# Kernel optimization log

Hardware: AMD Instinct MI355X
Metric: run time of the kernel (lower is better)

Reference implementation:

```python
import jax, jax.numpy as jnp
import numpy as np

IN_CH = 256
OUT_CH = 64
HEADS = 8


def setup_inputs() -> dict:
    key = jax.random.key(0)
    ks = jax.random.split(key, 7)
    N = 4096
    proj = OUT_CH * HEADS
    s_in = 1.0 / np.sqrt(IN_CH)
    return {
        "query_input": jax.random.normal(ks[0], (N, IN_CH), dtype=jnp.float32),
        "Wq": jax.random.uniform(ks[1], (proj, IN_CH), jnp.float32, -s_in, s_in),
        "bq": jax.random.uniform(ks[2], (proj,), jnp.float32, -s_in, s_in),
        "Wk": jax.random.uniform(ks[3], (proj, IN_CH), jnp.float32, -s_in, s_in),
        "bk": jax.random.uniform(ks[4], (proj,), jnp.float32, -s_in, s_in),
        "Wv": jax.random.uniform(ks[5], (proj, IN_CH), jnp.float32, -s_in, s_in),
        "bv": jax.random.uniform(ks[6], (proj,), jnp.float32, -s_in, s_in),
    }


def reference(query_input, Wq, bq, Wk, bk, Wv, bv):
    N = query_input.shape[0]
    # projections -> [N, H, M]
    q = (query_input @ Wq.T + bq).reshape(N, HEADS, OUT_CH)
    k = (query_input @ Wk.T + bk).reshape(N, HEADS, OUT_CH)
    v = (query_input @ Wv.T + bv).reshape(N, HEADS, OUT_CH)
    # sigmoid attention scores [N, L, H]
    attention_num = jax.nn.sigmoid(jnp.einsum('nhm,lhm->nlh', q, k))
    # sum-normalization over L (keys)
    normalizer = attention_num.sum(axis=1, keepdims=True)  # [N, 1, H]
    attention = attention_num / normalizer
    # weighted V reduction [N, H, D], then mean over heads -> [N, D]
    out = jnp.einsum('nlh,lhd->nhd', attention, v).mean(axis=1)
    return out
```

## Files before the change

### kernel.cpp

```cpp
#include <hip/hip_runtime.h>
#include <hip/hip_bf16.h>
#include <math.h>

#define N_TOK 4096
#define IN_CH 256
#define OUT_CH 64
#define HEADS 8
#define PROJ (OUT_CH * HEADS)
#define NLOG2E -1.44269504088896340736f

typedef float f32x4 __attribute__((ext_vector_type(4)));
typedef __bf16 bf16x8 __attribute__((ext_vector_type(8)));
typedef unsigned short ushort_t;

__device__ inline ushort_t bf16rne(float x) {
    unsigned u = __float_as_uint(x);
    unsigned r = (u + 0x7FFFu + ((u >> 16) & 1u)) >> 16;
    return (ushort_t)r;
}

__global__ __launch_bounds__(256) void cast_pack_kernel(
    const float* __restrict__ X,
    const float* __restrict__ Wq, const float* __restrict__ Wk,
    const float* __restrict__ Wv,
    ushort_t* __restrict__ Xa, ushort_t* __restrict__ Wp)
{
    const int i = blockIdx.x * 256 + threadIdx.x;
    const float* src;
    ushort_t* dst;
    float scale = 1.0f;
    if (i < 131072) {
        const int t = i & 15, quad = (i >> 4) & 3, k8 = (i >> 6) & 7, g = i >> 9;
        src = X + (size_t)(g * 16 + t) * IN_CH + k8 * 32 + quad * 8;
        dst = Xa + (size_t)i * 8;
    } else {
        const int j = i - 131072;
        const int z = j >> 14;
        const int r = j & 16383;
        const int cl = r & 15, quad = (r >> 4) & 3, k8 = (r >> 6) & 7, gc = r >> 9;
        const float* W = (z == 0) ? Wq : (z == 1) ? Wk : Wv;
        src = W + (size_t)(gc * 16 + cl) * IN_CH + k8 * 32 + quad * 8;
        dst = Wp + (size_t)z * 131072 * 8 + (size_t)r * 8;
        if (z == 0) scale = NLOG2E;
    }
    float4 a = *(const float4*)src;
    float4 b = *(const float4*)(src + 4);
    ushort_t pk[8];
    pk[0] = bf16rne(a.x * scale); pk[1] = bf16rne(a.y * scale);
    pk[2] = bf16rne(a.z * scale); pk[3] = bf16rne(a.w * scale);
    pk[4] = bf16rne(b.x * scale); pk[5] = bf16rne(b.y * scale);
    pk[6] = bf16rne(b.z * scale); pk[7] = bf16rne(b.w * scale);
    *(uint4*)dst = *(uint4*)pk;
}

__global__ __launch_bounds__(256) void proj_mfma_kernel(
    const ushort_t* __restrict__ Xa, const ushort_t* __restrict__ Wp,
    const float* __restrict__ bq, const float* __restrict__ bk,
    const float* __restrict__ bv,
    ushort_t* __restrict__ Qb, ushort_t* __restrict__ Kb,
    ushort_t* __restrict__ Vt)
{
    const int z = blockIdx.z;
    const float* bias = (z == 0) ? bq : (z == 1) ? bk : bv;
    const float bscale = (z == 0) ? NLOG2E : 1.0f;
    const int c0 = blockIdx.x * 64;
    const int n0 = blockIdx.y * 64;

    const int tid = threadIdx.x;
    const int w = tid >> 6;
    const int lane = tid & 63;
    const int l15 = lane & 15;
    const int quad = lane >> 4;

    __shared__ ushort_t Es[64 * 68];

    const ushort_t* xa = Xa + (size_t)(blockIdx.y * 4 + w) * 4096 + quad * 128 + l15 * 8;
    const ushort_t* wp0 = Wp + (size_t)z * 131072 * 8 +
                          (size_t)(blockIdx.x * 4) * 4096 + quad * 128 + l15 * 8;

    f32x4 acc[4] = {{0.f, 0.f, 0.f, 0.f}, {0.f, 0.f, 0.f, 0.f},
                    {0.f, 0.f, 0.f, 0.f}, {0.f, 0.f, 0.f, 0.f}};

#pragma unroll 2
    for (int k8 = 0; k8 < 8; ++k8) {
        bf16x8 a = *(const bf16x8*)(xa + k8 * 512);
#pragma unroll
        for (int f = 0; f < 4; ++f) {
            bf16x8 b = *(const bf16x8*)(wp0 + f * 4096 + k8 * 512);
            acc[f] = __builtin_amdgcn_mfma_f32_16x16x32_bf16(a, b, acc[f], 0, 0, 0);
        }
    }

    if (z < 2) {
#pragma unroll
        for (int f = 0; f < 4; ++f) {
            const float bb = bias[c0 + f * 16 + l15] * bscale;
#pragma unroll
            for (int r = 0; r < 4; ++r)
                Es[(w * 16 + quad * 4 + r) * 68 + f * 16 + l15] = bf16rne(acc[f][r] + bb);
        }
    } else {
#pragma unroll
        for (int f = 0; f < 4; ++f) {
            const float bb = bias[c0 + f * 16 + l15];
#pragma unroll
            for (int r = 0; r < 4; ++r)
                Es[(f * 16 + l15) * 68 + w * 16 + quad * 4 + r] = bf16rne(acc[f][r] + bb);
        }
    }
    __syncthreads();

    const int erow = tid >> 2;
    const int ecol = (tid & 3) * 16;
    uint4 pk0 = *(uint4*)&Es[erow * 68 + ecol];
    uint4 pk1 = *(uint4*)&Es[erow * 68 + ecol + 8];
    if (z < 2) {
        ushort_t* out = z ? Kb : Qb;
        ushort_t* p = &out[(size_t)(n0 + erow) * PROJ + c0 + ecol];
        *(uint4*)p = pk0;
        *(uint4*)(p + 8) = pk1;
    } else {
        ushort_t* p = &Vt[(size_t)(c0 + erow) * N_TOK + n0 + ecol];
        *(uint4*)p = pk0;
        *(uint4*)(p + 8) = pk1;
    }
}

__global__ __launch_bounds__(256, 4) void attn_kernel(
    const ushort_t* __restrict__ Qb, const ushort_t* __restrict__ Kb,
    const ushort_t* __restrict__ Vt,
    float* __restrict__ NUM, float* __restrict__ DEN)
{
    const int h = blockIdx.y;
    const int z = blockIdx.z;
    const int n0 = blockIdx.x * 64;
    const int tid = threadIdx.x;
    const int w = tid >> 6;
    const int lane = tid & 63;
    const int l15 = lane & 15;
    const int quad = lane >> 4;

    __shared__ ushort_t Ks[64 * 64];
    __shared__ ushort_t Vs[64 * 64];
    __shared__ ushort_t Ps[4][16 * 72];

    bf16x8 qb[2];
    {
        const ushort_t* base = Qb + (size_t)(n0 + w * 16 + l15) * PROJ + h * 64 + quad * 8;
        qb[0] = *(const bf16x8*)(base);
        qb[1] = *(const bf16x8*)(base + 32);
    }

    bf16x8 onesv;
#pragma unroll
    for (int j = 0; j < 8; ++j) onesv[j] = (__bf16)1.0f;

    f32x4 o[4] = {{0.f, 0.f, 0.f, 0.f}, {0.f, 0.f, 0.f, 0.f},
                  {0.f, 0.f, 0.f, 0.f}, {0.f, 0.f, 0.f, 0.f}};
    f32x4 dacc = {0.f, 0.f, 0.f, 0.f};

    const int srow = tid >> 2;
    const int sc2 = (tid & 3) * 2;
    const int sp0 = (sc2 ^ (srow & 7)) * 8;
    const int sp1 = ((sc2 + 1) ^ (srow & 7)) * 8;
    const int xm = l15 & 7;
    const int rofA = (quad ^ xm) * 8;
    const int rofB = ((4 + quad) ^ xm) * 8;

    const ushort_t* kgp = Kb + (size_t)h * 64 + sc2 * 8 +
                          (size_t)(z * 2048 + srow) * PROJ;
    const ushort_t* vgp = Vt + (size_t)h * 64 * N_TOK + (size_t)srow * N_TOK +
                          sc2 * 8 + z * 2048;

    uint4 kr0 = ((const uint4*)kgp)[0], kr1 = ((const uint4*)kgp)[1];
    uint4 vr0 = ((const uint4*)vgp)[0], vr1 = ((const uint4*)vgp)[1];

    for (int lt = 0; lt < 32; ++lt) {
        __syncthreads();
        *(uint4*)&Ks[srow * 64 + sp0] = kr0;
        *(uint4*)&Ks[srow * 64 + sp1] = kr1;
        *(uint4*)&Vs[srow * 64 + sp0] = vr0;
        *(uint4*)&Vs[srow * 64 + sp1] = vr1;
        __syncthreads();

        if (lt < 31) {
            kgp += 64 * PROJ;
            vgp += 64;
            kr0 = ((const uint4*)kgp)[0]; kr1 = ((const uint4*)kgp)[1];
            vr0 = ((const uint4*)vgp)[0]; vr1 = ((const uint4*)vgp)[1];
        }

        f32x4 s[4] = {{0.f, 0.f, 0.f, 0.f}, {0.f, 0.f, 0.f, 0.f},
                      {0.f, 0.f, 0.f, 0.f}, {0.f, 0.f, 0.f, 0.f}};
#pragma unroll
        for (int f = 0; f < 4; ++f) {
            bf16x8 ka = *(const bf16x8*)&Ks[(f * 16 + l15) * 64 + rofA];
            s[f] = __builtin_amdgcn_mfma_f32_16x16x32_bf16(ka, qb[0], s[f], 0, 0, 0);
        }
#pragma unroll
        for (int f = 0; f < 4; ++f) {
            bf16x8 ka = *(const bf16x8*)&Ks[(f * 16 + l15) * 64 + rofB];
            s[f] = __builtin_amdgcn_mfma_f32_16x16x32_bf16(ka, qb[1], s[f], 0, 0, 0);
        }

        ushort_t* pw = &Ps[w][l15 * 72];
#pragma unroll
        for (int f = 0; f < 4; ++f) {
            float p0 = __builtin_amdgcn_rcpf(1.0f + __builtin_amdgcn_exp2f(s[f][0]));
            float p1 = __builtin_amdgcn_rcpf(1.0f + __builtin_amdgcn_exp2f(s[f][1]));
            float p2 = __builtin_amdgcn_rcpf(1.0f + __builtin_amdgcn_exp2f(s[f][2]));
            float p3 = __builtin_amdgcn_rcpf(1.0f + __builtin_amdgcn_exp2f(s[f][3]));
            unsigned u0 = __float_as_uint(p0) + 0x8000u;
            unsigned u1 = __float_as_uint(p1) + 0x8000u;
            unsigned u2 = __float_as_uint(p2) + 0x8000u;
            unsigned u3 = __float_as_uint(p3) + 0x8000u;
            uint2 pk;
            pk.x = __builtin_amdgcn_perm(u1, u0, 0x07060302u);
            pk.y = __builtin_amdgcn_perm(u3, u2, 0x07060302u);
            *(uint2*)&pw[f * 16 + quad * 4] = pk;
        }

#pragma unroll
        for (int c = 0; c < 2; ++c) {
            bf16x8 pa = *(const bf16x8*)&Ps[w][l15 * 72 + c * 32 + quad * 8];
            const int rof = c ? rofB : rofA;
#pragma unroll
            for (int f = 0; f < 4; ++f) {
                bf16x8 vb = *(const bf16x8*)&Vs[(f * 16 + l15) * 64 + rof];
                o[f] = __builtin_amdgcn_mfma_f32_16x16x32_bf16(pa, vb, o[f], 0, 0, 0);
            }
            dacc = __builtin_amdgcn_mfma_f32_16x16x32_bf16(pa, onesv, dacc, 0, 0, 0);
        }
    }

#pragma unroll
    for (int f = 0; f < 4; ++f) {
#pragma unroll
        for (int r = 0; r < 4; ++r) {
            const int q = n0 + w * 16 + quad * 4 + r;
            NUM[((size_t)z * N_TOK + q) * PROJ + h * 64 + f * 16 + l15] = o[f][r];
        }
    }
    if (l15 == 0) {
#pragma unroll
        for (int r = 0; r < 4; ++r)
            DEN[((size_t)z * N_TOK + n0 + w * 16 + quad * 4 + r) * HEADS + h] = dacc[r];
    }
}

__global__ __launch_bounds__(256) void reduce_kernel(
    const float* __restrict__ NUM, const float* __restrict__ DEN,
    float* __restrict__ out)
{
    const int g = blockIdx.x * 256 + threadIdx.x;
    const int n = g >> 6;
    const int d = g & 63;
    float acc = 0.0f;
#pragma unroll
    for (int hh = 0; hh < HEADS; ++hh) {
        float num = NUM[(size_t)n * PROJ + hh * 64 + d] +
                    NUM[((size_t)N_TOK + n) * PROJ + hh * 64 + d];
        float dd = DEN[(size_t)n * HEADS + hh] +
                   DEN[((size_t)N_TOK + n) * HEADS + hh];
        acc += num / dd;
    }
    out[g] = acc * 0.125f;
}

extern "C" void kernel_launch(void* const* d_in, const int* in_sizes, int n_in,
                              void* d_out, int out_size, void* d_ws, size_t ws_size,
                              hipStream_t stream) {
    (void)in_sizes; (void)n_in; (void)out_size; (void)ws_size;
    const float* X  = (const float*)d_in[0];
    const float* Wq = (const float*)d_in[1];
    const float* bq = (const float*)d_in[2];
    const float* Wk = (const float*)d_in[3];
    const float* bk = (const float*)d_in[4];
    const float* Wv = (const float*)d_in[5];
    const float* bv = (const float*)d_in[6];
    float* out = (float*)d_out;

    float* NUM = (float*)d_ws;
    float* DEN = NUM + (size_t)2 * N_TOK * PROJ;
    ushort_t* Qb = (ushort_t*)(DEN + (size_t)2 * N_TOK * HEADS);
    ushort_t* Kb = Qb + (size_t)N_TOK * PROJ;
    ushort_t* Vt = Kb + (size_t)N_TOK * PROJ;
    ushort_t* Xa = Vt + (size_t)N_TOK * PROJ;
    ushort_t* Wp = Xa + (size_t)N_TOK * IN_CH;

    cast_pack_kernel<<<dim3(704), 256, 0, stream>>>(X, Wq, Wk, Wv, Xa, Wp);
    proj_mfma_kernel<<<dim3(PROJ / 64, N_TOK / 64, 3), 256, 0, stream>>>(
        Xa, Wp, bq, bk, bv, Qb, Kb, Vt);
    attn_kernel<<<dim3(N_TOK / 64, HEADS, 2), 256, 0, stream>>>(
        Qb, Kb, Vt, NUM, DEN);
    reduce_kernel<<<dim3(N_TOK * OUT_CH / 256), 256, 0, stream>>>(NUM, DEN, out);
}
```

Baseline: 142.9 us.

## Split attention keys four ways when workspace allows and raise MFMA wave priority

Templates the attention and reduce kernels on the number of key splits and picks four splits instead of two when the workspace is large enough. This doubles the grid to 2048 blocks and halves each block's key loop, so more blocks are in flight to hide latency. It also wraps the MFMA sections in s_setprio so matrix work gets issued ahead of other waves. The cost is twice as much partial NUM/DEN traffic to write and then reduce.

```diff
diff --git a/kernel.cpp b/kernel.cpp
--- a/kernel.cpp
+++ b/kernel.cpp
@@ -126,11 +126,15 @@
     }
 }
 
+template<int ZS>
 __global__ __launch_bounds__(256, 4) void attn_kernel(
     const ushort_t* __restrict__ Qb, const ushort_t* __restrict__ Kb,
     const ushort_t* __restrict__ Vt,
     float* __restrict__ NUM, float* __restrict__ DEN)
 {
+    constexpr int KEYS = N_TOK / ZS;
+    constexpr int TILES = KEYS / 64;
+
     const int h = blockIdx.y;
     const int z = blockIdx.z;
     const int n0 = blockIdx.x * 64;
@@ -168,14 +172,14 @@
     const int rofB = ((4 + quad) ^ xm) * 8;
 
     const ushort_t* kgp = Kb + (size_t)h * 64 + sc2 * 8 +
-                          (size_t)(z * 2048 + srow) * PROJ;
+                          (size_t)(z * KEYS + srow) * PROJ;
     const ushort_t* vgp = Vt + (size_t)h * 64 * N_TOK + (size_t)srow * N_TOK +
-                          sc2 * 8 + z * 2048;
+                          sc2 * 8 + z * KEYS;
 
     uint4 kr0 = ((const uint4*)kgp)[0], kr1 = ((const uint4*)kgp)[1];
     uint4 vr0 = ((const uint4*)vgp)[0], vr1 = ((const uint4*)vgp)[1];
 
-    for (int lt = 0; lt < 32; ++lt) {
+    for (int lt = 0; lt < TILES; ++lt) {
         __syncthreads();
         *(uint4*)&Ks[srow * 64 + sp0] = kr0;
         *(uint4*)&Ks[srow * 64 + sp1] = kr1;
@@ -183,7 +187,7 @@
         *(uint4*)&Vs[srow * 64 + sp1] = vr1;
         __syncthreads();
 
-        if (lt < 31) {
+        if (lt < TILES - 1) {
             kgp += 64 * PROJ;
             vgp += 64;
             kr0 = ((const uint4*)kgp)[0]; kr1 = ((const uint4*)kgp)[1];
@@ -192,6 +196,7 @@
 
         f32x4 s[4] = {{0.f, 0.f, 0.f, 0.f}, {0.f, 0.f, 0.f, 0.f},
                       {0.f, 0.f, 0.f, 0.f}, {0.f, 0.f, 0.f, 0.f}};
+        __builtin_amdgcn_s_setprio(1);
 #pragma unroll
         for (int f = 0; f < 4; ++f) {
             bf16x8 ka = *(const bf16x8*)&Ks[(f * 16 + l15) * 64 + rofA];
@@ -202,6 +207,7 @@
             bf16x8 ka = *(const bf16x8*)&Ks[(f * 16 + l15) * 64 + rofB];
             s[f] = __builtin_amdgcn_mfma_f32_16x16x32_bf16(ka, qb[1], s[f], 0, 0, 0);
         }
+        __builtin_amdgcn_s_setprio(0);
 
         ushort_t* pw = &Ps[w][l15 * 72];
 #pragma unroll
@@ -220,6 +226,7 @@
             *(uint2*)&pw[f * 16 + quad * 4] = pk;
         }
 
+        __builtin_amdgcn_s_setprio(1);
 #pragma unroll
         for (int c = 0; c < 2; ++c) {
             bf16x8 pa = *(const bf16x8*)&Ps[w][l15 * 72 + c * 32 + quad * 8];
@@ -231,6 +238,7 @@
             }
             dacc = __builtin_amdgcn_mfma_f32_16x16x32_bf16(pa, onesv, dacc, 0, 0, 0);
         }
+        __builtin_amdgcn_s_setprio(0);
     }
 
 #pragma unroll
@@ -248,6 +256,7 @@
     }
 }
 
+template<int ZS>
 __global__ __launch_bounds__(256) void reduce_kernel(
     const float* __restrict__ NUM, const float* __restrict__ DEN,
     float* __restrict__ out)
@@ -258,10 +267,12 @@
     float acc = 0.0f;
 #pragma unroll
     for (int hh = 0; hh < HEADS; ++hh) {
-        float num = NUM[(size_t)n * PROJ + hh * 64 + d] +
-                    NUM[((size_t)N_TOK + n) * PROJ + hh * 64 + d];
-        float dd = DEN[(size_t)n * HEADS + hh] +
-                   DEN[((size_t)N_TOK + n) * HEADS + hh];
+        float num = 0.0f, dd = 0.0f;
+#pragma unroll
+        for (int zz = 0; zz < ZS; ++zz) {
+            num += NUM[((size_t)zz * N_TOK + n) * PROJ + hh * 64 + d];
+            dd  += DEN[((size_t)zz * N_TOK + n) * HEADS + hh];
+        }
         acc += num / dd;
     }
     out[g] = acc * 0.125f;
@@ -270,7 +281,7 @@
 extern "C" void kernel_launch(void* const* d_in, const int* in_sizes, int n_in,
                               void* d_out, int out_size, void* d_ws, size_t ws_size,
                               hipStream_t stream) {
-    (void)in_sizes; (void)n_in; (void)out_size; (void)ws_size;
+    (void)in_sizes; (void)n_in; (void)out_size;
     const float* X  = (const float*)d_in[0];
     const float* Wq = (const float*)d_in[1];
     const float* bq = (const float*)d_in[2];
@@ -280,9 +291,15 @@
     const float* bv = (const float*)d_in[6];
     float* out = (float*)d_out;
 
+    const size_t NEED4 =
+        (size_t)4 * N_TOK * PROJ * 4 + (size_t)4 * N_TOK * HEADS * 4 +
+        (size_t)3 * N_TOK * PROJ * 2 + (size_t)N_TOK * IN_CH * 2 +
+        (size_t)3 * PROJ * IN_CH * 2;
+    const int ZS = (ws_size >= NEED4) ? 4 : 2;
+
     float* NUM = (float*)d_ws;
-    float* DEN = NUM + (size_t)2 * N_TOK * PROJ;
-    ushort_t* Qb = (ushort_t*)(DEN + (size_t)2 * N_TOK * HEADS);
+    float* DEN = NUM + (size_t)ZS * N_TOK * PROJ;
+    ushort_t* Qb = (ushort_t*)(DEN + (size_t)ZS * N_TOK * HEADS);
     ushort_t* Kb = Qb + (size_t)N_TOK * PROJ;
     ushort_t* Vt = Kb + (size_t)N_TOK * PROJ;
     ushort_t* Xa = Vt + (size_t)N_TOK * PROJ;
@@ -291,7 +308,15 @@
     cast_pack_kernel<<<dim3(704), 256, 0, stream>>>(X, Wq, Wk, Wv, Xa, Wp);
     proj_mfma_kernel<<<dim3(PROJ / 64, N_TOK / 64, 3), 256, 0, stream>>>(
         Xa, Wp, bq, bk, bv, Qb, Kb, Vt);
-    attn_kernel<<<dim3(N_TOK / 64, HEADS, 2), 256, 0, stream>>>(
-        Qb, Kb, Vt, NUM, DEN);
-    reduce_kernel<<<dim3(N_TOK * OUT_CH / 256), 256, 0, stream>>>(NUM, DEN, out);
-}
+    if (ZS == 4) {
+        attn_kernel<4><<<dim3(N_TOK / 64, HEADS, 4), 256, 0, stream>>>(
+            Qb, Kb, Vt, NUM, DEN);
+        reduce_kernel<4><<<dim3(N_TOK * OUT_CH / 256), 256, 0, stream>>>(
+            NUM, DEN, out);
+    } else {
+        attn_kernel<2><<<dim3(N_TOK / 64, HEADS, 2), 256, 0, stream>>>(
+            Qb, Kb, Vt, NUM, DEN);
+        reduce_kernel<2><<<dim3(N_TOK * OUT_CH / 256), 256, 0, stream>>>(
+            NUM, DEN, out);
+    }
+}
```

Result: no change. 142.8 us (-0.1%).
